# Kernel optimization log

Hardware: AMD Instinct MI355X
Metric: run time of the kernel (lower is better)

Reference implementation:

```python
import math
import jax, jax.numpy as jnp
import numpy as np

B, S, H = 4, 4096, 1024
NH, HD = 16, 64
MLP_DIM = 4096


def _gelu_tanh(x):
    c = math.sqrt(2.0 / math.pi)
    return 0.5 * x * (1.0 + jnp.tanh(c * (x + 0.044715 * x * x * x)))


def _layernorm(x, w, b, eps=1e-5):
    mu = jnp.mean(x, axis=-1, keepdims=True)
    var = jnp.var(x, axis=-1, keepdims=True)
    return (x - mu) * jax.lax.rsqrt(var + eps) * w + b


def setup_inputs() -> dict:
    key = jax.random.key(0)
    ks = jax.random.split(key, 12)
    s = 0.02
    return {
        "x": jax.random.normal(ks[0], (B, S, H), jnp.float32),
        "ln1_w": jnp.ones((H,), jnp.float32),
        "ln1_b": jnp.zeros((H,), jnp.float32),
        "q_w": jax.random.normal(ks[1], (H, H), jnp.float32) * s,
        "q_b": jnp.zeros((H,), jnp.float32),
        "k_w": jax.random.normal(ks[2], (H, H), jnp.float32) * s,
        "k_b": jnp.zeros((H,), jnp.float32),
        "v_w": jax.random.normal(ks[3], (H, H), jnp.float32) * s,
        "v_b": jnp.zeros((H,), jnp.float32),
        "o_w": jax.random.normal(ks[4], (H, H), jnp.float32) * s,
        "o_b": jnp.zeros((H,), jnp.float32),
        "ln2_w": jnp.ones((H,), jnp.float32),
        "ln2_b": jnp.zeros((H,), jnp.float32),
        "fc_w": jax.random.normal(ks[5], (H, MLP_DIM), jnp.float32) * s,
        "fc_b": jnp.zeros((MLP_DIM,), jnp.float32),
        "proj_w": jax.random.normal(ks[6], (MLP_DIM, H), jnp.float32) * (s / math.sqrt(2 * 12)),
        "proj_b": jnp.zeros((H,), jnp.float32),
    }


def reference(x, ln1_w, ln1_b, q_w, q_b, k_w, k_b, v_w, v_b, o_w, o_b,
              ln2_w, ln2_b, fc_w, fc_b, proj_w, proj_b):
    bsz, seqlen, h = x.shape
    ln_x = _layernorm(x, ln1_w, ln1_b)

    # projections -> [b, nh, t, hd]
    def heads(y):
        return y.reshape(bsz, seqlen, NH, HD).transpose(0, 2, 1, 3)

    q = heads(ln_x @ q_w + q_b)
    k = heads(ln_x @ k_w + k_b)
    v = heads(ln_x @ v_w + v_b)

    # feature map: elu(x)+1
    qf = jax.nn.elu(q) + 1.0
    kf = jax.nn.elu(k) + 1.0

    kv = jnp.einsum('bhtd,bhte->bhde', kf, v)              # [b,nh,hd,hd]
    norm = 1.0 / (jnp.einsum('bhtd,bhd->bht', qf, kf.sum(axis=2)) + 1e-6)
    out = jnp.einsum('bhtd,bhde->bhte', qf, kv) * norm[..., None]
    out = out.transpose(0, 2, 1, 3).reshape(bsz, seqlen, h)
    attn = out @ o_w + o_b

    x = x + attn
    h_mlp = _gelu_tanh(_layernorm(x, ln2_w, ln2_b) @ fc_w + fc_b)
    x = x + (h_mlp @ proj_w + proj_b)
    return x
```

## Files before the change

kernel.cpp:

```cpp
#include <hip/hip_runtime.h>
#include <hip/hip_bf16.h>
#include <cstdint>
#include <cstddef>

typedef __bf16 bf16;
typedef __bf16 bf16x8 __attribute__((ext_vector_type(8)));
typedef __bf16 bf16x4 __attribute__((ext_vector_type(4)));
typedef float  f32x4  __attribute__((ext_vector_type(4)));

typedef __attribute__((address_space(1))) void gvoid_t;
typedef __attribute__((address_space(3))) void lvoid_t;

#define GLD_LDS16(g, l) __builtin_amdgcn_global_load_lds( \
    (gvoid_t*)(uintptr_t)(g), (lvoid_t*)(uint32_t)(uintptr_t)(l), 16, 0, 0)

#define SBAR() __builtin_amdgcn_s_barrier()
#define SCHED_FENCE() __builtin_amdgcn_sched_barrier(0)
#define WAIT_VM0() asm volatile("s_waitcnt vmcnt(0)" ::: "memory")
#define WAIT_VM8() asm volatile("s_waitcnt vmcnt(8)" ::: "memory")
#define WAIT_LGKM0() asm volatile("s_waitcnt lgkmcnt(0)" ::: "memory")

__global__ __launch_bounds__(256) void transpose_cast(
    const float* __restrict__ in, bf16* __restrict__ out, int R, int C)
{
  __shared__ float tile[32][33];
  const int bx = blockIdx.x;
  const int by = blockIdx.y;
  const int tx = threadIdx.x;
  const int ty = threadIdx.y;
#pragma unroll
  for (int i = 0; i < 32; i += 8)
    tile[ty + i][tx] = in[(size_t)(by * 32 + ty + i) * C + bx * 32 + tx];
  __syncthreads();
#pragma unroll
  for (int i = 0; i < 32; i += 8)
    out[(size_t)(bx * 32 + ty + i) * R + by * 32 + tx] = (bf16)tile[tx][ty + i];
}

__global__ __launch_bounds__(256) void pack3(
    const float* __restrict__ a, const float* __restrict__ b,
    const float* __restrict__ c, float* __restrict__ o)
{
  const int i = blockIdx.x * 256 + threadIdx.x;
  o[i] = i < 1024 ? a[i] : (i < 2048 ? b[i - 1024] : c[i - 2048]);
}

__global__ __launch_bounds__(256) void ln_row(
    const float* __restrict__ x, const float* __restrict__ w,
    const float* __restrict__ b, bf16* __restrict__ out)
{
  const int row = blockIdx.x;
  const int tid = threadIdx.x;
  const float4 v = ((const float4*)(x + (size_t)row * 1024))[tid];
  float s  = v.x + v.y + v.z + v.w;
  float ss = v.x * v.x + v.y * v.y + v.z * v.z + v.w * v.w;
#pragma unroll
  for (int off = 32; off > 0; off >>= 1) {
    s  += __shfl_down(s, off);
    ss += __shfl_down(ss, off);
  }
  __shared__ float red[8];
  const int wid = tid >> 6, lane = tid & 63;
  if (lane == 0) { red[wid] = s; red[4 + wid] = ss; }
  __syncthreads();
  s  = red[0] + red[1] + red[2] + red[3];
  ss = red[4] + red[5] + red[6] + red[7];
  const float mu   = s * (1.f / 1024.f);
  const float var  = ss * (1.f / 1024.f) - mu * mu;
  const float rstd = rsqrtf(var + 1e-5f);
  const float4 wv = ((const float4*)w)[tid];
  const float4 bv = ((const float4*)b)[tid];
  bf16x4 ov;
  ov[0] = (bf16)((v.x - mu) * rstd * wv.x + bv.x);
  ov[1] = (bf16)((v.y - mu) * rstd * wv.y + bv.y);
  ov[2] = (bf16)((v.z - mu) * rstd * wv.z + bv.z);
  ov[3] = (bf16)((v.w - mu) * rstd * wv.w + bv.w);
  *(bf16x4*)(out + (size_t)row * 1024 + tid * 4) = ov;
}

template <int EPI>
__global__ __launch_bounds__(512, 2) void gemm256(
    const bf16* __restrict__ A, const bf16* __restrict__ BT,
    const float* __restrict__ bias, const float* __restrict__ resid,
    void* __restrict__ outp, int M, int N, int K, int nx)
{
  __shared__ __align__(16) char lds[131072];
  const int tid  = threadIdx.x;
  const int wid  = tid >> 6, lane = tid & 63;
  const int wr   = wid >> 2, wc = wid & 3;
  const int ln15 = lane & 15, lhi = lane >> 4;

  const int nwg = (int)gridDim.x;
  const int cpx = nwg >> 3;
  const int bid = (int)blockIdx.x;
  const int lg  = (bid & 7) * cpx + (bid >> 3);
  const int bx  = lg % nx, by = lg / nx;
  const int row0 = by << 8, col0 = bx << 8;

  const int srow  = tid >> 3;
  const int sslot = (tid & 7) ^ (srow & 7);
  const bf16* aS = A  + (size_t)(row0 + srow) * K + sslot * 8;
  const bf16* bS = BT + (size_t)(col0 + srow) * K + sslot * 8;
  const size_t rjump = (size_t)K << 6;
  char* ldsW = lds + wid * 1024;

  const int rAb = (wr << 7) + ln15;
  const int rBb = (wc << 6) + ln15;
  const int sl0 = lhi ^ (ln15 & 7);
  const int sl1 = (4 + lhi) ^ (ln15 & 7);
  const int aOff0 = rAb * 128 + sl0 * 16;
  const int aOff1 = rAb * 128 + sl1 * 16;
  const int bOff0 = rBb * 128 + sl0 * 16 + 65536;
  const int bOff1 = rBb * 128 + sl1 * 16 + 65536;

  f32x4 acc[8][4] = {};
  const int nt = K >> 6;

#define STG(D, KT) do { \
    const bf16* ga_ = aS + (size_t)(KT) * 64; \
    const bf16* gb_ = bS + (size_t)(KT) * 64; \
    char* la_ = ldsW + (D) * 32768; \
    char* lb_ = la_ + 65536; \
    GLD_LDS16(ga_,             la_);         GLD_LDS16(gb_,             lb_); \
    GLD_LDS16(ga_ + rjump,     la_ + 8192);  GLD_LDS16(gb_ + rjump,     lb_ + 8192); \
    GLD_LDS16(ga_ + 2 * rjump, la_ + 16384); GLD_LDS16(gb_ + 2 * rjump, lb_ + 16384); \
    GLD_LDS16(ga_ + 3 * rjump, la_ + 24576); GLD_LDS16(gb_ + 3 * rjump, lb_ + 24576); \
  } while (0)

  STG(0, 0);
  STG(1, 1);
  WAIT_VM8();
  SBAR();

  for (int kt = 0; kt < nt; ++kt) {
    const int d = kt & 1;
    const char* base = (const char*)lds + d * 32768;

    bf16x8 a0[8], b0[4], a1[8], b1[4];
#pragma unroll
    for (int m = 0; m < 8; ++m) a0[m] = *(const bf16x8*)(base + aOff0 + m * 2048);
#pragma unroll
    for (int n = 0; n < 4; ++n) b0[n] = *(const bf16x8*)(base + bOff0 + n * 2048);
#pragma unroll
    for (int m = 0; m < 8; ++m) a1[m] = *(const bf16x8*)(base + aOff1 + m * 2048);
#pragma unroll
    for (int n = 0; n < 4; ++n) b1[n] = *(const bf16x8*)(base + bOff1 + n * 2048);

    WAIT_LGKM0();
    SBAR();
    if (kt + 2 < nt) STG(d, kt + 2);
    SCHED_FENCE();

    __builtin_amdgcn_s_setprio(1);
#pragma unroll
    for (int m = 0; m < 8; ++m)
#pragma unroll
      for (int n = 0; n < 4; ++n)
        acc[m][n] = __builtin_amdgcn_mfma_f32_16x16x32_bf16(a0[m], b0[n], acc[m][n], 0, 0, 0);
#pragma unroll
    for (int m = 0; m < 8; ++m)
#pragma unroll
      for (int n = 0; n < 4; ++n)
        acc[m][n] = __builtin_amdgcn_mfma_f32_16x16x32_bf16(a1[m], b1[n], acc[m][n], 0, 0, 0);
    __builtin_amdgcn_s_setprio(0);

    if (kt + 2 < nt) { WAIT_VM8(); }
    else if (kt + 1 < nt) { WAIT_VM0(); }
    SBAR();
  }
#undef STG

  const int lr4 = lhi << 2;
#pragma unroll
  for (int m = 0; m < 8; ++m) {
#pragma unroll
    for (int n = 0; n < 4; ++n) {
      const int c_i = col0 + wc * 64 + n * 16 + ln15;
      const float bv = bias[c_i];
#pragma unroll
      for (int j = 0; j < 4; ++j) {
        const int r_i = row0 + wr * 128 + m * 16 + lr4 + j;
        const size_t idx = (size_t)r_i * N + c_i;
        float val = acc[m][n][j] + bv;
        if constexpr (EPI == 0) {
          ((bf16*)outp)[idx] = (bf16)val;
        } else if constexpr (EPI == 1) {
          ((bf16*)outp)[idx] = (bf16)(val > 0.f ? val + 1.f : __expf(val));
        } else if constexpr (EPI == 2) {
          ((float*)outp)[idx] = val + resid[idx];
        } else if constexpr (EPI == 3) {
          const float u  = 0.7978845608028654f * (val + 0.044715f * val * val * val);
          const float th = 1.f - 2.f / (__expf(2.f * u) + 1.f);
          ((bf16*)outp)[idx] = (bf16)(0.5f * val * (1.f + th));
        } else {
          if (c_i < 2048)
            ((bf16*)outp)[idx] = (bf16)(val > 0.f ? val + 1.f : __expf(val));
          else
            ((bf16*)outp)[idx] = (bf16)val;
        }
      }
    }
  }
}

__global__ __launch_bounds__(256) void kv_part_kernel(
    const bf16* __restrict__ qkv, float* __restrict__ kv_part,
    float* __restrict__ ksum_part)
{
  const int bh = blockIdx.x >> 3, ch = blockIdx.x & 7;
  const int b = bh >> 4, h = bh & 15;
  const int tid = threadIdx.x;
  const int e = tid & 63, dg = tid >> 6;
  const size_t grow0 = (size_t)b * 4096 + (size_t)ch * 512;
  const size_t kbase = 1024 + (size_t)h * 64;
  __shared__ bf16 skf[8][64], sv[8][64];
  float accum[16];
#pragma unroll
  for (int i = 0; i < 16; ++i) accum[i] = 0.f;
  float ks = 0.f;
  const int tt = tid >> 5, cc = (tid & 31) << 1;
  for (int t0 = 0; t0 < 512; t0 += 8) {
    __syncthreads();
    const size_t base = (grow0 + t0 + tt) * 3072 + kbase + cc;
    *(uint32_t*)&skf[tt][cc] = *(const uint32_t*)(qkv + base);
    *(uint32_t*)&sv[tt][cc]  = *(const uint32_t*)(qkv + base + 1024);
    __syncthreads();
#pragma unroll
    for (int q = 0; q < 8; ++q) {
      const float vv = (float)sv[q][e];
#pragma unroll
      for (int dd = 0; dd < 16; ++dd)
        accum[dd] += (float)skf[q][dg * 16 + dd] * vv;
    }
    if (tid < 64) {
#pragma unroll
      for (int q = 0; q < 8; ++q) ks += (float)skf[q][tid];
    }
  }
  float* op = kv_part + (size_t)blockIdx.x * 4096 + (size_t)(dg * 16) * 64 + e;
#pragma unroll
  for (int dd = 0; dd < 16; ++dd) op[dd * 64] = accum[dd];
  if (tid < 64) ksum_part[(size_t)blockIdx.x * 64 + tid] = ks;
}

__global__ __launch_bounds__(256) void kv_reduce(
    const float* __restrict__ kvp, const float* __restrict__ ksp,
    float* __restrict__ kvf, float* __restrict__ ksf)
{
  const int bh = blockIdx.x;
  const int tid = threadIdx.x;
  for (int i = tid; i < 4096; i += 256) {
    float s = 0.f;
#pragma unroll
    for (int ch = 0; ch < 8; ++ch) s += kvp[((size_t)bh * 8 + ch) * 4096 + i];
    kvf[(size_t)bh * 4096 + i] = s;
  }
  if (tid < 64) {
    float s = 0.f;
#pragma unroll
    for (int ch = 0; ch < 8; ++ch) s += ksp[((size_t)bh * 8 + ch) * 64 + tid];
    ksf[(size_t)bh * 64 + tid] = s;
  }
}

__global__ __launch_bounds__(256) void attn_out_kernel(
    const bf16* __restrict__ qkv, const float* __restrict__ kvf,
    const float* __restrict__ ksf, bf16* __restrict__ attn)
{
  const int bh = blockIdx.x >> 6, rb = blockIdx.x & 63;
  const int b = bh >> 4, h = bh & 15;
  const int tid = threadIdx.x;
  const int e = tid & 63, rbase = (tid >> 6) << 4;
  __shared__ __align__(16) bf16 sqf[64][64];
  __shared__ float sks[64];
  const size_t grow0 = (size_t)b * 4096 + (size_t)rb * 64;

  {
    const int rr = tid >> 2, c0 = (tid & 3) << 4;
    const bf16* src = qkv + (grow0 + rr) * 3072 + h * 64 + c0;
    *(bf16x8*)&sqf[rr][c0]     = *(const bf16x8*)src;
    *(bf16x8*)&sqf[rr][c0 + 8] = *(const bf16x8*)(src + 8);
  }
  if (tid < 64) sks[tid] = ksf[(size_t)bh * 64 + tid];

  float kcol[64];
#pragma unroll
  for (int d = 0; d < 64; ++d) kcol[d] = kvf[(size_t)bh * 4096 + d * 64 + e];

  __syncthreads();

  for (int rr = 0; rr < 16; ++rr) {
    const int r = rbase + rr;
    bf16x8 q8[8];
#pragma unroll
    for (int i = 0; i < 8; ++i) q8[i] = *(const bf16x8*)&sqf[r][i * 8];
    float sk = 0.f, sv = 0.f;
#pragma unroll
    for (int i = 0; i < 8; ++i)
#pragma unroll
      for (int jj = 0; jj < 8; ++jj) {
        const float qd = (float)q8[i][jj];
        sk += qd * sks[i * 8 + jj];
        sv += qd * kcol[i * 8 + jj];
      }
    attn[(grow0 + r) * 1024 + h * 64 + e] = (bf16)(sv / (sk + 1e-6f));
  }
}

extern "C" void kernel_launch(void* const* d_in, const int* in_sizes, int n_in,
                              void* d_out, int out_size, void* d_ws, size_t ws_size,
                              hipStream_t stream)
{
  const float* x    = (const float*)d_in[0];
  const float* ln1w = (const float*)d_in[1];
  const float* ln1b = (const float*)d_in[2];
  const float* qw   = (const float*)d_in[3];
  const float* qb   = (const float*)d_in[4];
  const float* kw   = (const float*)d_in[5];
  const float* kb   = (const float*)d_in[6];
  const float* vw   = (const float*)d_in[7];
  const float* vb   = (const float*)d_in[8];
  const float* ow   = (const float*)d_in[9];
  const float* ob   = (const float*)d_in[10];
  const float* ln2w = (const float*)d_in[11];
  const float* ln2b = (const float*)d_in[12];
  const float* fcw  = (const float*)d_in[13];
  const float* fcb  = (const float*)d_in[14];
  const float* pjw  = (const float*)d_in[15];
  const float* pjb  = (const float*)d_in[16];
  float* out = (float*)d_out;
  char* ws = (char*)d_ws;

  constexpr size_t O_LNX  = 0;
  constexpr size_t O_QKV  = 33554432;
  constexpr size_t O_HMLP = 0;
  constexpr size_t O_KVP  = 134217728;
  constexpr size_t O_KSP  = 142606336;
  constexpr size_t O_KVF  = 142737408;
  constexpr size_t O_KSF  = 143785984;
  constexpr size_t O_ATTN = 143802368;
  constexpr size_t O_LN2  = 177356800;
  constexpr size_t O_WQ   = 210911232;
  constexpr size_t O_WO   = 217202688;
  constexpr size_t O_WFC  = 219299840;
  constexpr size_t O_WPJ  = 227688448;

  bf16* lnx   = (bf16*)(ws + O_LNX);
  bf16* qkv   = (bf16*)(ws + O_QKV);
  bf16* hmlp  = (bf16*)(ws + O_HMLP);
  float* kvp  = (float*)(ws + O_KVP);
  float* qkvb = (float*)(ws + O_KVP);
  float* ksp  = (float*)(ws + O_KSP);
  float* kvf  = (float*)(ws + O_KVF);
  float* ksf  = (float*)(ws + O_KSF);
  bf16* attn  = (bf16*)(ws + O_ATTN);
  bf16* ln2h  = (bf16*)(ws + O_LN2);
  bf16* wqkvT = (bf16*)(ws + O_WQ);
  bf16* woT   = (bf16*)(ws + O_WO);
  bf16* wfcT  = (bf16*)(ws + O_WFC);
  bf16* wpjT  = (bf16*)(ws + O_WPJ);

  const dim3 tb(32, 8);
  transpose_cast<<<dim3(32, 32),  tb, 0, stream>>>(qw,  wqkvT,                1024, 1024);
  transpose_cast<<<dim3(32, 32),  tb, 0, stream>>>(kw,  wqkvT + 1024 * 1024,  1024, 1024);
  transpose_cast<<<dim3(32, 32),  tb, 0, stream>>>(vw,  wqkvT + 2048 * 1024,  1024, 1024);
  transpose_cast<<<dim3(32, 32),  tb, 0, stream>>>(ow,  woT, 1024, 1024);
  transpose_cast<<<dim3(128, 32), tb, 0, stream>>>(fcw, wfcT, 1024, 4096);
  transpose_cast<<<dim3(32, 128), tb, 0, stream>>>(pjw, wpjT, 4096, 1024);
  pack3<<<12, 256, 0, stream>>>(qb, kb, vb, qkvb);

  ln_row<<<16384, 256, 0, stream>>>(x, ln1w, ln1b, lnx);

  gemm256<4><<<768, 512, 0, stream>>>(lnx, wqkvT, qkvb, nullptr, qkv, 16384, 3072, 1024, 12);

  kv_part_kernel<<<512, 256, 0, stream>>>(qkv, kvp, ksp);
  kv_reduce<<<64, 256, 0, stream>>>(kvp, ksp, kvf, ksf);
  attn_out_kernel<<<4096, 256, 0, stream>>>(qkv, kvf, ksf, attn);

  gemm256<2><<<256, 512, 0, stream>>>(attn, woT, ob, x, out, 16384, 1024, 1024, 4);

  ln_row<<<16384, 256, 0, stream>>>(out, ln2w, ln2b, ln2h);

  gemm256<3><<<1024, 512, 0, stream>>>(ln2h, wfcT, fcb, nullptr, hmlp, 16384, 4096, 1024, 16);

  gemm256<2><<<256, 512, 0, stream>>>(hmlp, wpjT, pjb, out, out, 16384, 1024, 4096, 4);
}
```

Baseline: 715.2 us.

## Split GEMM k-step into four quadrant phases with interleaved staging and MFMA

```diff
diff --git a/kernel.cpp b/kernel.cpp
--- a/kernel.cpp
+++ b/kernel.cpp
@@ -16,8 +16,7 @@
 
 #define SBAR() __builtin_amdgcn_s_barrier()
 #define SCHED_FENCE() __builtin_amdgcn_sched_barrier(0)
-#define WAIT_VM0() asm volatile("s_waitcnt vmcnt(0)" ::: "memory")
-#define WAIT_VM8() asm volatile("s_waitcnt vmcnt(8)" ::: "memory")
+#define WAIT_VMN(n) asm volatile("s_waitcnt vmcnt(" #n ")" ::: "memory")
 #define WAIT_LGKM0() asm volatile("s_waitcnt lgkmcnt(0)" ::: "memory")
 
 __global__ __launch_bounds__(256) void transpose_cast(
@@ -97,78 +96,104 @@
   const int bx  = lg % nx, by = lg / nx;
   const int row0 = by << 8, col0 = bx << 8;
 
-  const int srow  = tid >> 3;
-  const int sslot = (tid & 7) ^ (srow & 7);
-  const bf16* aS = A  + (size_t)(row0 + srow) * K + sslot * 8;
-  const bf16* bS = BT + (size_t)(col0 + srow) * K + sslot * 8;
-  const size_t rjump = (size_t)K << 6;
-  char* ldsW = lds + wid * 1024;
-
-  const int rAb = (wr << 7) + ln15;
-  const int rBb = (wc << 6) + ln15;
-  const int sl0 = lhi ^ (ln15 & 7);
-  const int sl1 = (4 + lhi) ^ (ln15 & 7);
-  const int aOff0 = rAb * 128 + sl0 * 16;
-  const int aOff1 = rAb * 128 + sl1 * 16;
-  const int bOff0 = rBb * 128 + sl0 * 16 + 65536;
-  const int bOff1 = rBb * 128 + sl1 * 16 + 65536;
+  const int srowA = tid >> 3;
+  const int sslA  = (tid & 7) ^ (srowA & 7);
+  const bf16* aS  = A + (size_t)(row0 + srowA) * K + sslA * 8;
+  const size_t rjK = (size_t)K << 6;
+  const int u8    = tid >> 3, s8 = tid & 7;
+  const int gRowB = ((u8 >> 5) << 6) + (u8 & 31);
+  const int sslB  = s8 ^ (u8 & 7);
+  const bf16* bS  = BT + (size_t)(col0 + gRowB) * K + sslB * 8;
+
+  char* ldsAw = lds + wid * 1024;
+  char* ldsBw = lds + 65536 + wid * 1024;
+
+  const int slk0 = (lhi ^ (ln15 & 7)) << 4;
+  const int slk1 = ((4 + lhi) ^ (ln15 & 7)) << 4;
+  const int rowA0 = ((wr << 7) + ln15) * 128;
+  const int rowB0 = 65536 + (wc * 32 + ln15) * 128;
 
   f32x4 acc[8][4] = {};
+  bf16x8 a[4][2], b0[2][2], b1[2][2];
   const int nt = K >> 6;
 
-#define STG(D, KT) do { \
-    const bf16* ga_ = aS + (size_t)(KT) * 64; \
-    const bf16* gb_ = bS + (size_t)(KT) * 64; \
-    char* la_ = ldsW + (D) * 32768; \
-    char* lb_ = la_ + 65536; \
-    GLD_LDS16(ga_,             la_);         GLD_LDS16(gb_,             lb_); \
-    GLD_LDS16(ga_ + rjump,     la_ + 8192);  GLD_LDS16(gb_ + rjump,     lb_ + 8192); \
-    GLD_LDS16(ga_ + 2 * rjump, la_ + 16384); GLD_LDS16(gb_ + 2 * rjump, lb_ + 16384); \
-    GLD_LDS16(ga_ + 3 * rjump, la_ + 24576); GLD_LDS16(gb_ + 3 * rjump, lb_ + 24576); \
-  } while (0)
-
-  STG(0, 0);
-  STG(1, 1);
-  WAIT_VM8();
-  SBAR();
-
-  for (int kt = 0; kt < nt; ++kt) {
-    const int d = kt & 1;
-    const char* base = (const char*)lds + d * 32768;
-
-    bf16x8 a0[8], b0[4], a1[8], b1[4];
-#pragma unroll
-    for (int m = 0; m < 8; ++m) a0[m] = *(const bf16x8*)(base + aOff0 + m * 2048);
-#pragma unroll
-    for (int n = 0; n < 4; ++n) b0[n] = *(const bf16x8*)(base + bOff0 + n * 2048);
-#pragma unroll
-    for (int m = 0; m < 8; ++m) a1[m] = *(const bf16x8*)(base + aOff1 + m * 2048);
-#pragma unroll
-    for (int n = 0; n < 4; ++n) b1[n] = *(const bf16x8*)(base + bOff1 + n * 2048);
-
-    WAIT_LGKM0();
-    SBAR();
-    if (kt + 2 < nt) STG(d, kt + 2);
-    SCHED_FENCE();
-
-    __builtin_amdgcn_s_setprio(1);
-#pragma unroll
-    for (int m = 0; m < 8; ++m)
-#pragma unroll
-      for (int n = 0; n < 4; ++n)
-        acc[m][n] = __builtin_amdgcn_mfma_f32_16x16x32_bf16(a0[m], b0[n], acc[m][n], 0, 0, 0);
-#pragma unroll
-    for (int m = 0; m < 8; ++m)
-#pragma unroll
-      for (int n = 0; n < 4; ++n)
-        acc[m][n] = __builtin_amdgcn_mfma_f32_16x16x32_bf16(a1[m], b1[n], acc[m][n], 0, 0, 0);
-    __builtin_amdgcn_s_setprio(0);
-
-    if (kt + 2 < nt) { WAIT_VM8(); }
-    else if (kt + 1 < nt) { WAIT_VM0(); }
-    SBAR();
-  }
-#undef STG
+#define STG_A(D, KT, I) GLD_LDS16(aS + (size_t)(I) * rjK + (size_t)(KT) * 64, \
+                                  ldsAw + (D) * 32768 + (I) * 8192)
+#define STG_B(D, KT, NH, J) GLD_LDS16(bS + (size_t)((J) * 128 + (NH) * 32) * K + (size_t)(KT) * 64, \
+                                      ldsBw + (D) * 32768 + (NH) * 16384 + (J) * 8192)
+#define RD_A(D, MH) do { _Pragma("unroll") \
+    for (int m_ = 0; m_ < 4; ++m_) { \
+      a[m_][0] = *(const bf16x8*)(lds + (D) * 32768 + rowA0 + (MH) * 8192 + m_ * 2048 + slk0); \
+      a[m_][1] = *(const bf16x8*)(lds + (D) * 32768 + rowA0 + (MH) * 8192 + m_ * 2048 + slk1); \
+    } } while (0)
+#define RD_B(D, NH, DST) do { _Pragma("unroll") \
+    for (int n_ = 0; n_ < 2; ++n_) { \
+      DST[n_][0] = *(const bf16x8*)(lds + (D) * 32768 + rowB0 + (NH) * 16384 + n_ * 2048 + slk0); \
+      DST[n_][1] = *(const bf16x8*)(lds + (D) * 32768 + rowB0 + (NH) * 16384 + n_ * 2048 + slk1); \
+    } } while (0)
+#define MFMA8(MH, NH, BSRC) do { \
+    __builtin_amdgcn_s_setprio(1); \
+    _Pragma("unroll") for (int m_ = 0; m_ < 4; ++m_) \
+    _Pragma("unroll") for (int n_ = 0; n_ < 2; ++n_) { \
+      acc[(MH) * 4 + m_][(NH) * 2 + n_] = __builtin_amdgcn_mfma_f32_16x16x32_bf16( \
+          a[m_][0], BSRC[n_][0], acc[(MH) * 4 + m_][(NH) * 2 + n_], 0, 0, 0); \
+      acc[(MH) * 4 + m_][(NH) * 2 + n_] = __builtin_amdgcn_mfma_f32_16x16x32_bf16( \
+          a[m_][1], BSRC[n_][1], acc[(MH) * 4 + m_][(NH) * 2 + n_], 0, 0, 0); \
+    } \
+    __builtin_amdgcn_s_setprio(0); } while (0)
+
+  STG_A(0, 0, 0); STG_A(0, 0, 2);
+  STG_B(0, 0, 0, 0); STG_B(0, 0, 0, 1);
+  STG_B(0, 0, 1, 0); STG_B(0, 0, 1, 1);
+  STG_A(0, 0, 1); STG_A(0, 0, 3);
+  WAIT_VMN(0);
+  SBAR(); SCHED_FENCE();
+
+  for (int kt = 0; kt < nt - 1; ++kt) {
+    const int d = kt & 1, dn = d ^ 1;
+    RD_A(d, 0); RD_B(d, 0, b0);
+    STG_A(dn, kt + 1, 0); STG_A(dn, kt + 1, 2);
+    SBAR(); WAIT_LGKM0(); SCHED_FENCE();
+    MFMA8(0, 0, b0);
+    SBAR(); SCHED_FENCE();
+    RD_B(d, 1, b1);
+    STG_B(dn, kt + 1, 0, 0); STG_B(dn, kt + 1, 0, 1);
+    WAIT_VMN(4);
+    SBAR(); WAIT_LGKM0(); SCHED_FENCE();
+    MFMA8(0, 1, b1);
+    SBAR(); SCHED_FENCE();
+    RD_A(d, 1);
+    STG_B(dn, kt + 1, 1, 0); STG_B(dn, kt + 1, 1, 1);
+    SBAR(); WAIT_LGKM0(); SCHED_FENCE();
+    MFMA8(1, 0, b0);
+    SBAR(); SCHED_FENCE();
+    STG_A(dn, kt + 1, 1); STG_A(dn, kt + 1, 3);
+    MFMA8(1, 1, b1);
+    WAIT_VMN(2);
+    SBAR(); SCHED_FENCE();
+  }
+
+  {
+    const int d = (nt - 1) & 1;
+    RD_A(d, 0); RD_B(d, 0, b0);
+    SBAR(); WAIT_LGKM0(); SCHED_FENCE();
+    MFMA8(0, 0, b0);
+    SBAR(); SCHED_FENCE();
+    RD_B(d, 1, b1);
+    WAIT_VMN(0);
+    SBAR(); WAIT_LGKM0(); SCHED_FENCE();
+    MFMA8(0, 1, b1);
+    SBAR(); SCHED_FENCE();
+    RD_A(d, 1);
+    WAIT_LGKM0(); SCHED_FENCE();
+    MFMA8(1, 0, b0);
+    MFMA8(1, 1, b1);
+  }
+#undef STG_A
+#undef STG_B
+#undef RD_A
+#undef RD_B
+#undef MFMA8
 
   const int lr4 = lhi << 2;
 #pragma unroll
@@ -361,9 +386,9 @@
   bf16* wpjT  = (bf16*)(ws + O_WPJ);
 
   const dim3 tb(32, 8);
-  transpose_cast<<<dim3(32, 32),  tb, 0, stream>>>(qw,  wqkvT,                1024, 1024);
-  transpose_cast<<<dim3(32, 32),  tb, 0, stream>>>(kw,  wqkvT + 1024 * 1024,  1024, 1024);
-  transpose_cast<<<dim3(32, 32),  tb, 0, stream>>>(vw,  wqkvT + 2048 * 1024,  1024, 1024);
+  transpose_cast<<<dim3(32, 32),  tb, 0, stream>>>(qw,  wqkvT,               1024, 1024);
+  transpose_cast<<<dim3(32, 32),  tb, 0, stream>>>(kw,  wqkvT + 1024 * 1024, 1024, 1024);
+  transpose_cast<<<dim3(32, 32),  tb, 0, stream>>>(vw,  wqkvT + 2048 * 1024, 1024, 1024);
   transpose_cast<<<dim3(32, 32),  tb, 0, stream>>>(ow,  woT, 1024, 1024);
   transpose_cast<<<dim3(128, 32), tb, 0, stream>>>(fcw, wfcT, 1024, 4096);
   transpose_cast<<<dim3(32, 128), tb, 0, stream>>>(pjw, wpjT, 4096, 1024);
```

New measurement: 701.9 us. Within noise of the previous version (-1.9%).
